# Performance work log

Hardware: AMD Instinct MI355X
Metric: run time of the kernel (lower is better)

## Reference

```python
import jax, jax.numpy as jnp
import numpy as np
from jax import lax

MID = 64      # mid_size -> token seq len = MID*MID = 4096
DM = 64       # d_model = in_channels
DI = 128      # d_inner = expand * d_model
DS = 16       # d_state
DC = 4        # d_conv
DTR = 4       # dt_rank = ceil(DM/16)
EPS = 1e-5


def conv3x3(x, w):
    return lax.conv_general_dilated(x, w, (1, 1), ((1, 1), (1, 1)),
                                    dimension_numbers=('NCHW', 'OIHW', 'NCHW'))


def layernorm(x, w, b):
    mu = jnp.mean(x, -1, keepdims=True)
    var = jnp.mean((x - mu) ** 2, -1, keepdims=True)
    return (x - mu) * lax.rsqrt(var + EPS) * w + b


def bilinear(x, h, w):
    b, c = x.shape[:2]
    return jax.image.resize(x, (b, c, h, w), method='bilinear', antialias=False)


def mamba(tok, in_w, conv_w, conv_b, xproj_w, dt_w, dt_b, Alog, D, out_w):
    # tok: (b, L, DM)
    b, L, _ = tok.shape
    xz = tok @ in_w.T                                # (b, L, 2*DI)
    xc, z = jnp.split(xz, 2, axis=-1)
    # causal depthwise conv1d over sequence
    xcT = xc.transpose(0, 2, 1)                      # (b, DI, L)
    xconv = lax.conv_general_dilated(xcT, conv_w, (1,), ((DC - 1, 0),),
                                     dimension_numbers=('NCH', 'OIH', 'NCH'),
                                     feature_group_count=DI)
    xconv = xconv + conv_b[None, :, None]
    u = jax.nn.silu(xconv.transpose(0, 2, 1))        # (b, L, DI)
    x_dbl = u @ xproj_w.T                            # (b, L, DTR+2*DS)
    dt, B, C = jnp.split(x_dbl, [DTR, DTR + DS], axis=-1)
    dt = jax.nn.softplus(dt @ dt_w.T + dt_b)         # (b, L, DI)
    A = -jnp.exp(Alog)                               # (DI, DS)
    dA = jnp.exp(dt[..., None] * A)                  # (b, L, DI, DS)
    dBu = dt[..., None] * B[:, :, None, :] * u[..., None]

    def step(h, xs):
        a_t, bu_t = xs
        h = a_t * h + bu_t
        return h, h

    h0 = jnp.zeros((b, DI, DS), dt.dtype)
    _, hs = lax.scan(step, h0, (dA.transpose(1, 0, 2, 3), dBu.transpose(1, 0, 2, 3)))
    y = jnp.einsum('lbns,bls->bln', hs, C) + u * D   # (b, L, DI)
    y = y * jax.nn.silu(z)
    return y @ out_w.T                               # (b, L, DM)


def setup_inputs() -> dict:
    key = jax.random.key(0)
    ks = iter(jax.random.split(key, 32))
    s = 0.02
    d = {}
    d['x'] = jax.random.normal(next(ks), (4, 64, 128, 128), jnp.float32)
    for n, shp in [('cb_w1', (64, 64, 3, 3)), ('cb_w2', (64, 64, 3, 3)),
                   ('sm_w1', (64, 64, 3, 3)), ('sm_w2', (64, 64, 3, 3))]:
        d[n] = jax.random.normal(next(ks), shp, jnp.float32) * s
    d['ln1_w'] = jnp.ones((DM,), jnp.float32); d['ln1_b'] = jnp.zeros((DM,), jnp.float32)
    d['ln2_w'] = jnp.ones((DM,), jnp.float32); d['ln2_b'] = jnp.zeros((DM,), jnp.float32)
    for p in ['m1', 'm2']:
        d[p + '_in_w'] = jax.random.normal(next(ks), (2 * DI, DM), jnp.float32) * s
        d[p + '_conv_w'] = jax.random.normal(next(ks), (DI, 1, DC), jnp.float32) * s
        d[p + '_conv_b'] = jnp.zeros((DI,), jnp.float32)
        d[p + '_xproj_w'] = jax.random.normal(next(ks), (DTR + 2 * DS, DI), jnp.float32) * s
        d[p + '_dt_w'] = jax.random.normal(next(ks), (DI, DTR), jnp.float32) * s
        d[p + '_dt_b'] = jnp.full((DI,), -2.0, jnp.float32)
        d[p + '_Alog'] = jnp.broadcast_to(jnp.log(jnp.arange(1, DS + 1, dtype=jnp.float32)), (DI, DS)).copy()
        d[p + '_D'] = jnp.ones((DI,), jnp.float32)
        d[p + '_out_w'] = jax.random.normal(next(ks), (DM, DI), jnp.float32) * s
    return d


def reference(x, cb_w1, cb_w2, ln1_w, ln1_b, ln2_w, ln2_b,
              m1_in_w, m1_conv_w, m1_conv_b, m1_xproj_w, m1_dt_w, m1_dt_b, m1_Alog, m1_D, m1_out_w,
              m2_in_w, m2_conv_w, m2_conv_b, m2_xproj_w, m2_dt_w, m2_dt_b, m2_Alog, m2_D, m2_out_w,
              sm_w1, sm_w2):
    b, c, h, w = x.shape
    xr = conv3x3(jax.nn.relu(conv3x3(x, cb_w1)), cb_w2) + x
    x_small = xr if (h, w) == (MID, MID) else bilinear(xr, MID, MID)
    tokens = x_small.reshape(b, c, MID * MID).transpose(0, 2, 1)   # (b, L, c)
    main = mamba(layernorm(tokens, ln1_w, ln1_b),
                 m1_in_w, m1_conv_w, m1_conv_b, m1_xproj_w, m1_dt_w, m1_dt_b, m1_Alog, m1_D, m1_out_w)
    gate_feat = mamba(layernorm(tokens, ln2_w, ln2_b),
                      m2_in_w, m2_conv_w, m2_conv_b, m2_xproj_w, m2_dt_w, m2_dt_b, m2_Alog, m2_D, m2_out_w)
    gate = jax.nn.softmax(gate_feat, axis=1)                       # softmax over token dim
    tokens = tokens + gate * main
    feat = tokens.transpose(0, 2, 1).reshape(b, c, MID, MID)
    if (h, w) != (MID, MID):
        feat = bilinear(feat, h, w)
    return conv3x3(jax.nn.relu(conv3x3(feat, sm_w1)), sm_w2)
```

## Files before the change

### kernel.cpp

```cpp
#include <hip/hip_runtime.h>

typedef unsigned int u32;
typedef unsigned short u16;
typedef __attribute__((ext_vector_type(8))) short short8;
typedef __attribute__((ext_vector_type(4))) float f32x4;

__device__ __forceinline__ float sigmoidf_(float x){
  return 1.f / (1.f + __expf(-x));
}
__device__ __forceinline__ u16 f2bf(float f){
  union { float f; u32 i; } v; v.f = f;
  u32 r = v.i + 0x7fffu + ((v.i >> 16) & 1u);
  return (u16)(r >> 16);
}
__device__ __forceinline__ float bf2f(u32 u){
  union { float f; u32 i; } v; v.i = (u & 0xffffu) << 16; return v.f;
}
__device__ __forceinline__ float softplus_(float x){
  return fmaxf(x, 0.f) + __logf(1.f + __expf(-fabsf(x)));
}

__global__ __launch_bounds__(256) void k_setup(
    const float* __restrict__ w0, u16* __restrict__ h0, u16* __restrict__ l0,
    const float* __restrict__ w1, u16* __restrict__ h1, u16* __restrict__ l1,
    const float* __restrict__ w2, u16* __restrict__ h2, u16* __restrict__ l2,
    const float* __restrict__ w3, u16* __restrict__ h3, u16* __restrict__ l3,
    const float* __restrict__ Wa, const float* __restrict__ lnwa, const float* __restrict__ lnba,
    float* __restrict__ W2a, float* __restrict__ B2a,
    const float* __restrict__ Wb, const float* __restrict__ lnwb, const float* __restrict__ lnbb,
    float* __restrict__ W2b, float* __restrict__ B2b,
    const float* __restrict__ src, u16* __restrict__ PH, u16* __restrict__ PL,
    u16* __restrict__ BPH, u16* __restrict__ BPL)
{
  __shared__ float ld[64 * 129];
  int bx = blockIdx.x;
  int tid = threadIdx.x;
  if (bx < 577){
    int gidx = bx * 256 + tid;
    if (gidx < 147456){
      int set = gidx / 36864;
      int idx = gidx - set * 36864;
      const float* w; u16* WH; u16* WL;
      if (set == 0){ w = w0; WH = h0; WL = l0; }
      else if (set == 1){ w = w1; WH = h1; WL = l1; }
      else if (set == 2){ w = w2; WH = h2; WL = l2; }
      else { w = w3; WH = h3; WL = l3; }
      int j    = idx & 7;
      int lane = (idx >> 3) & 63;
      int nt   = (idx >> 9) & 3;
      int kc   = (idx >> 11) & 1;
      int t    = idx >> 12;
      int ic = kc * 32 + ((lane >> 4) & 3) * 8 + j;
      int oc = nt * 16 + (lane & 15);
      float v = w[(oc * 64 + ic) * 9 + t];
      u16 h = f2bf(v);
      u16 l = f2bf(v - bf2f(h));
      WH[idx] = h; WL[idx] = l;
    } else {
      int i = gidx - 147456;
      if (i >= 128) return;
      int m = i >> 6, j = i & 63;
      const float* W   = m ? Wb   : Wa;
      const float* lnw = m ? lnwb : lnwa;
      const float* lnb = m ? lnbb : lnba;
      float* W2 = m ? W2b : W2a;
      float* B2 = m ? B2b : B2a;
      float bias = 0.f;
#pragma unroll
      for (int k4 = 0; k4 < 16; k4++){
        float4 wv = *(const float4*)&W[j * 64 + k4 * 4];
        float4 gw = *(const float4*)&lnw[k4 * 4];
        float4 gb = *(const float4*)&lnb[k4 * 4];
        W2[j * 64 + k4 * 4 + 0] = wv.x * gw.x;
        W2[j * 64 + k4 * 4 + 1] = wv.y * gw.y;
        W2[j * 64 + k4 * 4 + 2] = wv.z * gw.z;
        W2[j * 64 + k4 * 4 + 3] = wv.w * gw.w;
        bias = fmaf(wv.x, gb.x, bias);
        bias = fmaf(wv.y, gb.y, bias);
        bias = fmaf(wv.z, gb.z, bias);
        bias = fmaf(wv.w, gb.w, bias);
      }
      B2[j] = bias;
    }
  } else {
    int bid2 = bx - 577;
    int yp = bid2 % 130;
    int b  = bid2 / 130;
    int ys = yp - 1;
    if (yp == 0 || yp == 129){
      for (int i = tid; i < 130 * 64; i += 256){
        int x = i >> 6, c = i & 63;
        size_t o = (((size_t)b * 130 + yp) * 130 + x) * 64 + c;
        BPH[o] = 0; BPL[o] = 0;
      }
    } else {
      for (int i = tid; i < 128; i += 256){
        int x = (i >= 64) ? 129 : 0, c = i & 63;
        size_t o = (((size_t)b * 130 + yp) * 130 + x) * 64 + c;
        BPH[o] = 0; BPL[o] = 0;
      }
    }
    if ((u32)ys < 128u){
      for (int i = tid; i < 8192; i += 256){
        int c = i >> 7, x = i & 127;
        ld[c * 129 + x] = src[((size_t)(b * 64 + c) * 128 + ys) * 128 + x];
      }
    }
    __syncthreads();
    for (int i = tid; i < 130 * 64; i += 256){
      int xp = i >> 6, c = i & 63;
      float v = 0.f;
      if ((u32)ys < 128u && (u32)(xp - 1) < 128u) v = ld[c * 129 + (xp - 1)];
      u16 h = f2bf(v);
      u16 l = f2bf(v - bf2f(h));
      size_t o = (((size_t)b * 130 + yp) * 130 + xp) * 64 + c;
      PH[o] = h; PL[o] = l;
    }
  }
}

__global__ __launch_bounds__(256) void k_prepup(const float* __restrict__ FEAT,
                                                u16* __restrict__ PH, u16* __restrict__ PL,
                                                u16* __restrict__ BPH, u16* __restrict__ BPL){
  __shared__ float ld0[64 * 65], ld1[64 * 65];
  int yp = blockIdx.x;
  int b  = blockIdx.y;
  int ys = yp - 1;
  int tid = threadIdx.x;
  if (yp == 0 || yp == 129){
    for (int i = tid; i < 130 * 64; i += 256){
      int x = i >> 6, c = i & 63;
      size_t o = (((size_t)b * 130 + yp) * 130 + x) * 64 + c;
      BPH[o] = 0; BPL[o] = 0;
    }
  } else {
    for (int i = tid; i < 128; i += 256){
      int x = (i >= 64) ? 129 : 0, c = i & 63;
      size_t o = (((size_t)b * 130 + yp) * 130 + x) * 64 + c;
      BPH[o] = 0; BPL[o] = 0;
    }
  }
  float wy = 0.f;
  if ((u32)ys < 128u){
    float ay = 0.5f * ys - 0.25f;
    int fy = (int)floorf(ay); wy = ay - fy;
    int y0s = fy < 0 ? 0 : fy, y1s = fy + 1 > 63 ? 63 : fy + 1;
    for (int i = tid; i < 1024; i += 256){
      int c = i >> 4, x4 = (i & 15) * 4;
      float4 a0 = *(const float4*)&FEAT[((size_t)(b * 64 + c) * 64 + y0s) * 64 + x4];
      float4 a1 = *(const float4*)&FEAT[((size_t)(b * 64 + c) * 64 + y1s) * 64 + x4];
      ld0[c * 65 + x4 + 0] = a0.x; ld0[c * 65 + x4 + 1] = a0.y;
      ld0[c * 65 + x4 + 2] = a0.z; ld0[c * 65 + x4 + 3] = a0.w;
      ld1[c * 65 + x4 + 0] = a1.x; ld1[c * 65 + x4 + 1] = a1.y;
      ld1[c * 65 + x4 + 2] = a1.z; ld1[c * 65 + x4 + 3] = a1.w;
    }
  }
  __syncthreads();
  for (int i = tid; i < 130 * 64; i += 256){
    int xp = i >> 6, c = i & 63;
    float v = 0.f;
    int xs = xp - 1;
    if ((u32)ys < 128u && (u32)xs < 128u){
      float ax = 0.5f * xs - 0.25f;
      int fx = (int)floorf(ax); float wx = ax - fx;
      int x0s = fx < 0 ? 0 : fx, x1s = fx + 1 > 63 ? 63 : fx + 1;
      float v0 = (1.f - wx) * ld0[c * 65 + x0s] + wx * ld0[c * 65 + x1s];
      float v1 = (1.f - wx) * ld1[c * 65 + x0s] + wx * ld1[c * 65 + x1s];
      v = (1.f - wy) * v0 + wy * v1;
    }
    u16 h = f2bf(v);
    u16 l = f2bf(v - bf2f(h));
    size_t o = (((size_t)b * 130 + yp) * 130 + xp) * 64 + c;
    PH[o] = h; PL[o] = l;
  }
}

__global__ __launch_bounds__(256) void k_convm(
    const u16* __restrict__ PH, const u16* __restrict__ PL,
    const u16* __restrict__ WH, const u16* __restrict__ WL,
    const float* __restrict__ resid,
    u16* __restrict__ OBH, u16* __restrict__ OBL,
    float* __restrict__ OUTF, float* __restrict__ T, float* __restrict__ NT,
    int mode)
{
  __shared__ __align__(16) u32 smem[9024];
  u16* Ah_s = (u16*)smem;
  u16* Al_s = Ah_s + 5760;
  int tid = threadIdx.x;
  int lane = tid & 63, w = tid >> 6;
  int quad = lane >> 4, lcol = lane & 15;
  int b = blockIdx.z, y0 = blockIdx.y * 8, x0 = blockIdx.x * 16;

  f32x4 acc[2][4];
#pragma unroll
  for (int mt = 0; mt < 2; mt++)
#pragma unroll
    for (int nt = 0; nt < 4; nt++)
      acc[mt][nt] = (f32x4){0.f, 0.f, 0.f, 0.f};

  for (int kc = 0; kc < 2; kc++){
    __syncthreads();
    for (int i = tid; i < 720; i += 256){
      int q = i & 3;
      int rc = i >> 2;
      int r = rc / 18, c = rc - r * 18;
      size_t so = (((size_t)b * 130 + y0 + r) * 130 + (x0 + c)) * 64 + kc * 32 + q * 8;
      int de = (r * 18 + c) * 32 + q * 8;
      *(uint4*)(Ah_s + de) = *(const uint4*)(PH + so);
      *(uint4*)(Al_s + de) = *(const uint4*)(PL + so);
    }
    __syncthreads();
#pragma unroll
    for (int t = 0; t < 9; t++){
      int dy = t / 3, dx = t - dy * 3;
      short8 bh[4], bl[4];
#pragma unroll
      for (int nt = 0; nt < 4; nt++){
        int o = ((t * 2 + kc) * 4 + nt) * 512 + lane * 8;
        bh[nt] = *(const short8*)(WH + o);
        bl[nt] = *(const short8*)(WL + o);
      }
      short8 ah[2], al[2];
#pragma unroll
      for (int mt = 0; mt < 2; mt++){
        int e = ((w * 2 + mt + dy) * 18 + (lcol + dx)) * 32 + quad * 8;
        ah[mt] = *(const short8*)(Ah_s + e);
        al[mt] = *(const short8*)(Al_s + e);
      }
#pragma unroll
      for (int mt = 0; mt < 2; mt++)
#pragma unroll
        for (int nt = 0; nt < 4; nt++){
          acc[mt][nt] = __builtin_amdgcn_mfma_f32_16x16x32_bf16(ah[mt], bh[nt], acc[mt][nt], 0, 0, 0);
          acc[mt][nt] = __builtin_amdgcn_mfma_f32_16x16x32_bf16(ah[mt], bl[nt], acc[mt][nt], 0, 0, 0);
          acc[mt][nt] = __builtin_amdgcn_mfma_f32_16x16x32_bf16(al[mt], bh[nt], acc[mt][nt], 0, 0, 0);
        }
    }
  }

  __syncthreads();
  if (mode == 0){
    u32* epi = smem;
#pragma unroll
    for (int mt = 0; mt < 2; mt++){
      int row = w * 2 + mt;
#pragma unroll
      for (int nt = 0; nt < 4; nt++){
#pragma unroll
        for (int reg = 0; reg < 4; reg++){
          float v = fmaxf(acc[mt][nt][reg], 0.f);
          u32 h = f2bf(v);
          u32 l = f2bf(v - bf2f(h));
          int ccol = quad * 4 + reg;
          int oc = nt * 16 + lcol;
          epi[(row * 16 + ccol) * 66 + oc] = h | (l << 16);
        }
      }
    }
    __syncthreads();
    for (int i = tid; i < 8192; i += 256){
      int px = i >> 6, oc = i & 63;
      int row = px >> 4, ccol = px & 15;
      u32 pk = epi[px * 66 + oc];
      size_t o = (((size_t)b * 130 + y0 + row + 1) * 130 + (x0 + ccol + 1)) * 64 + oc;
      OBH[o] = (u16)pk;
      OBL[o] = (u16)(pk >> 16);
    }
  } else {
    float* epi = (float*)smem;
#pragma unroll
    for (int mt = 0; mt < 2; mt++){
      int row = w * 2 + mt;
#pragma unroll
      for (int nt = 0; nt < 4; nt++){
#pragma unroll
        for (int reg = 0; reg < 4; reg++){
          int px = row * 16 + quad * 4 + reg;
          int oc = nt * 16 + lcol;
          epi[oc * 131 + px] = acc[mt][nt][reg];
        }
      }
    }
    __syncthreads();
    if (mode == 1){
      for (int i = tid; i < 8192; i += 256){
        int oc = i >> 7, px = i & 127;
        int row = px >> 4, c = px & 15;
        size_t o = (((size_t)b * 64 + oc) * 128 + y0 + row) * 128 + x0 + c;
        float v = epi[oc * 131 + px];
        if (resid) v += resid[o];
        OUTF[o] = v;
      }
    } else {
      for (int i = tid; i < 8192; i += 256){
        int oc = i >> 7, px = i & 127;
        int row = px >> 4, c = px & 15;
        size_t o = (((size_t)b * 64 + oc) * 128 + y0 + row) * 128 + x0 + c;
        epi[oc * 131 + px] += resid[o];
      }
      __syncthreads();
      float* redS  = (float*)smem + 8384;
      float* redQ  = redS + 288;
      float* stats = redQ + 288;
      int token = tid & 31, cgrp = tid >> 5;
      int tr = token >> 3, tc = token & 7;
      float av[8]; float s = 0.f, q = 0.f;
      int p0 = (2 * tr) * 16 + 2 * tc;
#pragma unroll
      for (int j = 0; j < 8; j++){
        int c = cgrp * 8 + j;
        const float* ep = epi + c * 131;
        float v = 0.25f * (ep[p0] + ep[p0 + 1] + ep[p0 + 16] + ep[p0 + 17]);
        av[j] = v; s += v; q = fmaf(v, v, q);
      }
      redS[token * 9 + cgrp] = s;
      redQ[token * 9 + cgrp] = q;
      __syncthreads();
      if (tid < 32){
        float S = 0.f, Q = 0.f;
        for (int g = 0; g < 8; g++){ S += redS[tid * 9 + g]; Q += redQ[tid * 9 + g]; }
        float mu = S * (1.f / 64.f);
        float var = Q * (1.f / 64.f) - mu * mu;
        stats[tid * 2] = mu;
        stats[tid * 2 + 1] = rsqrtf(var + 1e-5f);
      }
      __syncthreads();
      float mu = stats[token * 2], inv = stats[token * 2 + 1];
      int l = (blockIdx.y * 4 + tr) * 64 + blockIdx.x * 8 + tc;
      size_t to = ((size_t)b * 4096 + l) * 64 + cgrp * 8;
#pragma unroll
      for (int j = 0; j < 8; j++){
        T[to + j] = av[j];
        NT[to + j] = (av[j] - mu) * inv;
      }
    }
  }
}

__global__ __launch_bounds__(256) void k_inprojdw(
    const float* __restrict__ NT,
    const float* __restrict__ W2a, const float* __restrict__ B2a,
    float* __restrict__ Ua, float* __restrict__ Za,
    const float* __restrict__ cwa, const float* __restrict__ cba,
    const float* __restrict__ W2b, const float* __restrict__ B2b,
    float* __restrict__ Ub, float* __restrict__ Zb,
    const float* __restrict__ cwb, const float* __restrict__ cbb)
{
  __shared__ float wL[64 * 68];
  __shared__ float xcs[67 * 68];
  int mz = blockIdx.z;
  const float* W2 = mz ? W2b : W2a;
  const float* B2 = mz ? B2b : B2a;
  float* U = mz ? Ub : Ua;
  float* Z  = mz ? Zb : Za;
  const float* cw = mz ? cwb : cwa;
  const float* cb = mz ? cbb : cba;
  int tid = threadIdx.x;
  int t0 = blockIdx.x * 64;
  int j0 = blockIdx.y * 64;
  for (int i = tid; i < 4096; i += 256){
    int jl = i >> 6, k = i & 63;
    wL[jl * 68 + k] = W2[(size_t)(j0 + jl) * 64 + k];
  }
  __syncthreads();
  int tq = tid >> 4, cg = tid & 15;
  const float* ntp = NT + (size_t)(t0 + tq * 4) * 64;
  float acc[4][4];
#pragma unroll
  for (int c = 0; c < 4; c++){
    float bias = B2[j0 + cg + c * 16];
#pragma unroll
    for (int t = 0; t < 4; t++) acc[t][c] = bias;
  }
#pragma unroll 4
  for (int k4 = 0; k4 < 16; k4++){
    float4 lv[4];
#pragma unroll
    for (int t = 0; t < 4; t++)
      lv[t] = *(const float4*)(ntp + t * 64 + k4 * 4);
    float4 wv[4];
#pragma unroll
    for (int c = 0; c < 4; c++)
      wv[c] = *(const float4*)&wL[(cg + c * 16) * 68 + k4 * 4];
#pragma unroll
    for (int t = 0; t < 4; t++)
#pragma unroll
      for (int c = 0; c < 4; c++){
        acc[t][c] = fmaf(lv[t].x, wv[c].x, acc[t][c]);
        acc[t][c] = fmaf(lv[t].y, wv[c].y, acc[t][c]);
        acc[t][c] = fmaf(lv[t].z, wv[c].z, acc[t][c]);
        acc[t][c] = fmaf(lv[t].w, wv[c].w, acc[t][c]);
      }
  }
  if (j0 < 128){
    int isStart = ((t0 & 4095) == 0);
    if (tid < 192){
      int e = tid >> 6, col = tid & 63;
      float v = 0.f;
      if (!isStart){
        const float* np = NT + (size_t)(t0 - 3 + e) * 64;
        float a2 = B2[j0 + col];
#pragma unroll 4
        for (int k = 0; k < 64; k += 4){
          float4 nv = *(const float4*)(np + k);
          float4 wv = *(const float4*)&wL[col * 68 + k];
          a2 = fmaf(nv.x, wv.x, fmaf(nv.y, wv.y, fmaf(nv.z, wv.z, fmaf(nv.w, wv.w, a2))));
        }
        v = a2;
      }
      xcs[e * 68 + col] = v;
    }
#pragma unroll
    for (int t = 0; t < 4; t++)
#pragma unroll
      for (int c = 0; c < 4; c++)
        xcs[(3 + tq * 4 + t) * 68 + cg + c * 16] = acc[t][c];
    __syncthreads();
#pragma unroll
    for (int c = 0; c < 4; c++){
      int lc = cg + c * 16;
      int ch = j0 + lc;
      float4 wv = *(const float4*)(cw + ch * 4);
      float bias = cb[ch];
#pragma unroll
      for (int t = 0; t < 4; t++){
        int row = 3 + tq * 4 + t;
        float a = bias;
        a = fmaf(wv.w, xcs[row * 68 + lc], a);
        a = fmaf(wv.z, xcs[(row - 1) * 68 + lc], a);
        a = fmaf(wv.y, xcs[(row - 2) * 68 + lc], a);
        a = fmaf(wv.x, xcs[(row - 3) * 68 + lc], a);
        size_t tg = t0 + tq * 4 + t;
        U[tg * 128 + ch] = a * sigmoidf_(a);
      }
    }
  } else {
#pragma unroll
    for (int t = 0; t < 4; t++){
      size_t tg = t0 + tq * 4 + t;
#pragma unroll
      for (int c = 0; c < 4; c++)
        Z[tg * 128 + (j0 - 128) + cg + c * 16] = acc[t][c];
    }
  }
}

__global__ __launch_bounds__(256) void k_xprojdt(
    const float* __restrict__ U0, const float* __restrict__ XW0, float* __restrict__ DBL0,
    const float* __restrict__ U1, const float* __restrict__ XW1, float* __restrict__ DBL1)
{
  __shared__ float xw[36 * 132];
  int bid = blockIdx.x;
  int m = bid >> 7, blk = bid & 127;
  const float* Up   = m ? U1   : U0;
  const float* XWp  = m ? XW1  : XW0;
  float* DBLp = m ? DBL1 : DBL0;
  int tid = threadIdx.x;
  for (int i = tid; i < 4608; i += 256)
    xw[(i >> 7) * 132 + (i & 127)] = XWp[i];
  __syncthreads();
  int slot = tid >> 2, jq = tid & 3;
  size_t tgA = (size_t)blk * 128 + slot;
  size_t tgB = tgA + 64;
  const float4* upA = (const float4*)(Up + tgA * 128);
  const float4* upB = (const float4*)(Up + tgB * 128);
  float accA[9], accB[9];
#pragma unroll
  for (int jj = 0; jj < 9; jj++){ accA[jj] = 0.f; accB[jj] = 0.f; }
  for (int k4 = 0; k4 < 32; k4++){
    float4 uA = upA[k4];
    float4 uB = upB[k4];
#pragma unroll
    for (int jj = 0; jj < 9; jj++){
      float4 w = *(const float4*)&xw[(jq * 9 + jj) * 132 + k4 * 4];
      accA[jj] = fmaf(w.x, uA.x, fmaf(w.y, uA.y, fmaf(w.z, uA.z, fmaf(w.w, uA.w, accA[jj]))));
      accB[jj] = fmaf(w.x, uB.x, fmaf(w.y, uB.y, fmaf(w.z, uB.z, fmaf(w.w, uB.w, accB[jj]))));
    }
  }
#pragma unroll
  for (int jj = 0; jj < 9; jj++){
    DBLp[tgA * 36 + jq * 9 + jj] = accA[jj];
    DBLp[tgB * 36 + jq * 9 + jj] = accB[jj];
  }
}

__global__ __launch_bounds__(256) void k_scanA(
    const float* __restrict__ DBL0, const float* __restrict__ U0, const float* __restrict__ AL0,
    const float* __restrict__ DTW0, const float* __restrict__ DTB0,
    const float* __restrict__ DBL1, const float* __restrict__ U1, const float* __restrict__ AL1,
    const float* __restrict__ DTW1, const float* __restrict__ DTB1,
    float* __restrict__ HF, float* __restrict__ AP)
{
  __shared__ float su[32 * 65], sB[16 * 36], sdtr[128];
  int bid = blockIdx.x;
  int cg = bid & 1;
  int c  = (bid >> 1) & 127;
  int b  = (bid >> 8) & 3;
  int m  = bid >> 10;
  const float* DBLp = m ? DBL1 : DBL0;
  const float* Up   = m ? U1   : U0;
  const float* ALp  = m ? AL1  : AL0;
  const float* DTWp = m ? DTW1 : DTW0;
  const float* DTBp = m ? DTB1 : DTB0;
  int tid = threadIdx.x;
  int lane = tid & 63, w = tid >> 6;
  int lcol = lane & 15, q = lane >> 4;
  int chL = w * 16 + lcol;
  int n = cg * 64 + chL;
  size_t base = (size_t)b * 4096 + c * 32;
  for (int i = tid; i < 2048; i += 256){
    int ch = i & 63, l = i >> 6;
    su[l * 65 + ch] = Up[(base + l) * 128 + cg * 64 + ch];
  }
  for (int i = tid; i < 512; i += 256){
    int s = i & 15, l = i >> 4;
    sB[s * 36 + l] = DBLp[(base + l) * 36 + 4 + s];
  }
  if (tid < 128){
    int l = tid >> 2, jj = tid & 3;
    sdtr[tid] = DBLp[(base + l) * 36 + jj];
  }
  const float LOG2E = 1.4426950408889634f;
  float A1[4];
  bool fastp = true;
#pragma unroll
  for (int j = 0; j < 4; j++){
    A1[j] = -__expf(ALp[n * 16 + q * 4 + j]) * LOG2E;
    float expe = -(float)(q * 4 + j + 1) * LOG2E;
    fastp = fastp && (fabsf(A1[j] - expe) <= 1e-3f);
  }
  float4 wdt = *(const float4*)(DTWp + n * 4);
  float bdt = DTBp[n];
  __syncthreads();
  float h[4] = {0.f, 0.f, 0.f, 0.f};
  float ap[4] = {1.f, 1.f, 1.f, 1.f};
#pragma unroll
  for (int l4 = 0; l4 < 8; l4++){
    int lq = l4 * 4 + q;
    float4 dq = *(const float4*)&sdtr[lq * 4];
    float xq = bdt;
    xq = fmaf(wdt.x, dq.x, xq); xq = fmaf(wdt.y, dq.y, xq);
    xq = fmaf(wdt.z, dq.z, xq); xq = fmaf(wdt.w, dq.w, xq);
    float dtq = softplus_(xq);
    float rq = __expf(-dtq);
    float dts[4], rs[4];
    dts[0] = __shfl(dtq, lcol);       rs[0] = __shfl(rq, lcol);
    dts[1] = __shfl(dtq, lcol + 16);  rs[1] = __shfl(rq, lcol + 16);
    dts[2] = __shfl(dtq, lcol + 32);  rs[2] = __shfl(rq, lcol + 32);
    dts[3] = __shfl(dtq, lcol + 48);  rs[3] = __shfl(rq, lcol + 48);
    float4 Bv[4];
#pragma unroll
    for (int j = 0; j < 4; j++) Bv[j] = *(const float4*)&sB[(q * 4 + j) * 36 + l4 * 4];
    if (fastp){
#pragma unroll
      for (int jj = 0; jj < 4; jj++){
        int l = l4 * 4 + jj;
        float dt = dts[jj], r = rs[jj];
        float u  = su[l * 65 + chL];
        float dtu = dt * u;
        float r2 = r * r, r4 = r2 * r2;
        float r8 = r4 * r4;
        float p0 = (q == 0) ? r : (q == 1) ? r4 * r : (q == 2) ? r8 * r : (r8 * r4) * r;
        float a0 = p0, a1 = a0 * r, a2 = a1 * r, a3 = a2 * r;
        h[0] = fmaf(a0, h[0], dtu * (&Bv[0].x)[jj]); ap[0] *= a0;
        h[1] = fmaf(a1, h[1], dtu * (&Bv[1].x)[jj]); ap[1] *= a1;
        h[2] = fmaf(a2, h[2], dtu * (&Bv[2].x)[jj]); ap[2] *= a2;
        h[3] = fmaf(a3, h[3], dtu * (&Bv[3].x)[jj]); ap[3] *= a3;
      }
    } else {
#pragma unroll
      for (int jj = 0; jj < 4; jj++){
        int l = l4 * 4 + jj;
        float dt = dts[jj];
        float u  = su[l * 65 + chL];
        float dtu = dt * u;
#pragma unroll
        for (int j = 0; j < 4; j++){
          float a = exp2f(dt * A1[j]);
          h[j] = fmaf(a, h[j], dtu * (&Bv[j].x)[jj]);
          ap[j] *= a;
        }
      }
    }
  }
  size_t o = ((size_t)((m * 4 + b) * 128 + c)) * 2048 + n * 16 + q * 4;
  *(float4*)&HF[o] = make_float4(h[0], h[1], h[2], h[3]);
  *(float4*)&AP[o] = make_float4(ap[0], ap[1], ap[2], ap[3]);
}

__global__ __launch_bounds__(256) void k_scanB(
    const float* __restrict__ HF, const float* __restrict__ AP, float* __restrict__ HIN)
{
  int gid = blockIdx.x * 256 + threadIdx.x;
  int r = gid >> 3;
  int seg = gid & 7;
  int q = r >> 11;
  int p = r & 2047;
  size_t base = (size_t)q * 128 * 2048 + p + (size_t)seg * 16 * 2048;
  float a[16], f[16];
#pragma unroll
  for (int c8 = 0; c8 < 2; c8++){
#pragma unroll
    for (int j = 0; j < 8; j++){
      size_t o = base + (size_t)(c8 * 8 + j) * 2048;
      a[c8 * 8 + j] = AP[o];
      f[c8 * 8 + j] = HF[o];
    }
  }
  float A = 1.f, F = 0.f;
#pragma unroll
  for (int j = 0; j < 16; j++){ F = fmaf(a[j], F, f[j]); A *= a[j]; }
#pragma unroll
  for (int d = 1; d < 8; d <<= 1){
    float Au = __shfl_up(A, d, 8);
    float Fu = __shfl_up(F, d, 8);
    if (seg >= d){ F = fmaf(A, Fu, F); A = A * Au; }
  }
  float hin = __shfl_up(F, 1, 8);
  float h = (seg == 0) ? 0.f : hin;
#pragma unroll
  for (int j = 0; j < 16; j++){
    size_t o = base + (size_t)j * 2048;
    HIN[o] = h;
    h = fmaf(a[j], h, f[j]);
  }
}

__global__ __launch_bounds__(256) void k_scanC(
    const float* __restrict__ DBL0, const float* __restrict__ U0, const float* __restrict__ AL0,
    const float* __restrict__ DTW0, const float* __restrict__ DTB0,
    const float* __restrict__ D0, float* __restrict__ Y0,
    const float* __restrict__ DBL1, const float* __restrict__ U1, const float* __restrict__ AL1,
    const float* __restrict__ DTW1, const float* __restrict__ DTB1,
    const float* __restrict__ D1, float* __restrict__ Y1,
    const float* __restrict__ HIN)
{
  __shared__ float su[32 * 65], sB[16 * 36], sC[16 * 36], sdtr[128];
  int bid = blockIdx.x;
  int cg = bid & 1;
  int c  = (bid >> 1) & 127;
  int b  = (bid >> 8) & 3;
  int m  = bid >> 10;
  const float* DBLp = m ? DBL1 : DBL0;
  const float* Up   = m ? U1   : U0;
  const float* ALp  = m ? AL1  : AL0;
  const float* DTWp = m ? DTW1 : DTW0;
  const float* DTBp = m ? DTB1 : DTB0;
  const float* Dp   = m ? D1   : D0;
  float*       Yp   = m ? Y1   : Y0;
  int tid = threadIdx.x;
  int lane = tid & 63, w = tid >> 6;
  int lcol = lane & 15, q = lane >> 4;
  int chL = w * 16 + lcol;
  int n = cg * 64 + chL;
  size_t base = (size_t)b * 4096 + c * 32;
  for (int i = tid; i < 2048; i += 256){
    int ch = i & 63, l = i >> 6;
    su[l * 65 + ch] = Up[(base + l) * 128 + cg * 64 + ch];
  }
  for (int i = tid; i < 512; i += 256){
    int s = i & 15, l = i >> 4;
    size_t ob = (base + l) * 36;
    sB[s * 36 + l] = DBLp[ob + 4 + s];
    sC[s * 36 + l] = DBLp[ob + 20 + s];
  }
  if (tid < 128){
    int l = tid >> 2, jj = tid & 3;
    sdtr[tid] = DBLp[(base + l) * 36 + jj];
  }
  const float LOG2E = 1.4426950408889634f;
  float A1[4];
  bool fastp = true;
#pragma unroll
  for (int j = 0; j < 4; j++){
    A1[j] = -__expf(ALp[n * 16 + q * 4 + j]) * LOG2E;
    float expe = -(float)(q * 4 + j + 1) * LOG2E;
    fastp = fastp && (fabsf(A1[j] - expe) <= 1e-3f);
  }
  float4 wdt = *(const float4*)(DTWp + n * 4);
  float bdt = DTBp[n];
  float Dn = Dp[n];
  float4 hv = *(const float4*)&HIN[((size_t)((m * 4 + b) * 128 + c)) * 2048 + n * 16 + q * 4];
  float h[4] = {hv.x, hv.y, hv.z, hv.w};
  __syncthreads();
#pragma unroll
  for (int l4 = 0; l4 < 8; l4++){
    int lq = l4 * 4 + q;
    float4 dq = *(const float4*)&sdtr[lq * 4];
    float xq = bdt;
    xq = fmaf(wdt.x, dq.x, xq); xq = fmaf(wdt.y, dq.y, xq);
    xq = fmaf(wdt.z, dq.z, xq); xq = fmaf(wdt.w, dq.w, xq);
    float dtq = softplus_(xq);
    float rq = __expf(-dtq);
    float dts[4], rs[4];
    dts[0] = __shfl(dtq, lcol);       rs[0] = __shfl(rq, lcol);
    dts[1] = __shfl(dtq, lcol + 16);  rs[1] = __shfl(rq, lcol + 16);
    dts[2] = __shfl(dtq, lcol + 32);  rs[2] = __shfl(rq, lcol + 32);
    dts[3] = __shfl(dtq, lcol + 48);  rs[3] = __shfl(rq, lcol + 48);
    float4 Bv[4], Cv[4];
#pragma unroll
    for (int j = 0; j < 4; j++){
      Bv[j] = *(const float4*)&sB[(q * 4 + j) * 36 + l4 * 4];
      Cv[j] = *(const float4*)&sC[(q * 4 + j) * 36 + l4 * 4];
    }
    if (fastp){
#pragma unroll
      for (int jj = 0; jj < 4; jj++){
        int l = l4 * 4 + jj;
        float dt = dts[jj], r = rs[jj];
        float u  = su[l * 65 + chL];
        float dtu = dt * u;
        float r2 = r * r, r4 = r2 * r2;
        float r8 = r4 * r4;
        float p0 = (q == 0) ? r : (q == 1) ? r4 * r : (q == 2) ? r8 * r : (r8 * r4) * r;
        float a0 = p0, a1 = a0 * r, a2 = a1 * r, a3 = a2 * r;
        float p = 0.f;
        h[0] = fmaf(a0, h[0], dtu * (&Bv[0].x)[jj]); p = fmaf(h[0], (&Cv[0].x)[jj], p);
        h[1] = fmaf(a1, h[1], dtu * (&Bv[1].x)[jj]); p = fmaf(h[1], (&Cv[1].x)[jj], p);
        h[2] = fmaf(a2, h[2], dtu * (&Bv[2].x)[jj]); p = fmaf(h[2], (&Cv[2].x)[jj], p);
        h[3] = fmaf(a3, h[3], dtu * (&Bv[3].x)[jj]); p = fmaf(h[3], (&Cv[3].x)[jj], p);
        p += __shfl_xor(p, 16);
        p += __shfl_xor(p, 32);
        if (q == 0)
          Yp[(base + l) * 128 + n] = fmaf(u, Dn, p);
      }
    } else {
#pragma unroll
      for (int jj = 0; jj < 4; jj++){
        int l = l4 * 4 + jj;
        float dt = dts[jj];
        float u  = su[l * 65 + chL];
        float dtu = dt * u;
        float p = 0.f;
#pragma unroll
        for (int j = 0; j < 4; j++){
          float a = exp2f(dt * A1[j]);
          h[j] = fmaf(a, h[j], dtu * (&Bv[j].x)[jj]);
          p = fmaf(h[j], (&Cv[j].x)[jj], p);
        }
        p += __shfl_xor(p, 16);
        p += __shfl_xor(p, 32);
        if (q == 0)
          Yp[(base + l) * 128 + n] = fmaf(u, Dn, p);
      }
    }
  }
}

__global__ __launch_bounds__(256) void k_outproj(
    const float* __restrict__ Y0, const float* __restrict__ Zg0,
    const float* __restrict__ W0, float* __restrict__ OUT0,
    const float* __restrict__ Y1, const float* __restrict__ Zg1,
    const float* __restrict__ W1, float* __restrict__ OUT1,
    float* __restrict__ P)
{
  __shared__ float yl[16 * 128];
  __shared__ float wT[128 * 65];
  __shared__ float rM[256], rS[256];
  int m = blockIdx.y;
  const float* Y  = m ? Y1  : Y0;
  const float* Zg = m ? Zg1 : Zg0;
  const float* W  = m ? W1  : W0;
  float* OUT = m ? OUT1 : OUT0;
  int tid = threadIdx.x;
  size_t t0 = (size_t)blockIdx.x * 16;
  for (int i = tid; i < 2048; i += 256){
    float z = Zg[t0 * 128 + i];
    yl[i] = Y[t0 * 128 + i] * (z * sigmoidf_(z));
  }
  for (int i = tid; i < 8192; i += 256){
    int k = i & 127, j = i >> 7;
    wT[k * 65 + j] = W[j * 128 + k];
  }
  __syncthreads();
  int j = tid & 63;
  int tg = tid >> 6;
  float acc[4] = {0.f, 0.f, 0.f, 0.f};
  for (int k = 0; k < 128; k += 4){
    float w0 = wT[k * 65 + j], w1 = wT[(k+1) * 65 + j];
    float w2 = wT[(k+2) * 65 + j], w3 = wT[(k+3) * 65 + j];
#pragma unroll
    for (int t = 0; t < 4; t++){
      float4 yv = *(const float4*)&yl[(tg * 4 + t) * 128 + k];
      acc[t] = fmaf(w0, yv.x, fmaf(w1, yv.y, fmaf(w2, yv.z, fmaf(w3, yv.w, acc[t]))));
    }
  }
#pragma unroll
  for (int t = 0; t < 4; t++)
    OUT[(t0 + tg * 4 + t) * 64 + j] = acc[t];
  if (m == 1){
    float mx = fmaxf(fmaxf(acc[0], acc[1]), fmaxf(acc[2], acc[3]));
    float sm = __expf(acc[0] - mx) + __expf(acc[1] - mx) + __expf(acc[2] - mx) + __expf(acc[3] - mx);
    rM[tid] = mx; rS[tid] = sm;
    __syncthreads();
    if (tid < 64){
      float M = rM[tid], S = rS[tid];
      for (int p2 = 1; p2 < 4; p2++){
        float m2 = rM[p2 * 64 + tid], s2 = rS[p2 * 64 + tid];
        float Mn = fmaxf(M, m2);
        S = S * __expf(M - Mn) + s2 * __expf(m2 - Mn);
        M = Mn;
      }
      P[((size_t)blockIdx.x * 64 + tid) * 2] = M;
      P[((size_t)blockIdx.x * 64 + tid) * 2 + 1] = S;
    }
  }
}

__global__ void k_combine(const float* __restrict__ T, const float* __restrict__ MAIN,
                          const float* __restrict__ G, const float* __restrict__ P,
                          float* __restrict__ FEAT){
  int bid = blockIdx.x;
  int b = bid >> 6, row = bid & 63;
  int tid = threadIdx.x;
  __shared__ float tile[64 * 65];
  __shared__ float sM[256], sS[256], Mv[64], iSv[64];
  {
    int j2 = tid & 63, part = tid >> 6;
    float M = -3.4e38f, S = 0.f;
    for (int i = 0; i < 64; i++){
      int pb = part + i * 4;
      int idx = ((b * 256 + pb) * 64 + j2) * 2;
      float m2 = P[idx], s2 = P[idx + 1];
      float Mn = fmaxf(M, m2);
      S = S * __expf(M - Mn) + s2 * __expf(m2 - Mn);
      M = Mn;
    }
    sM[tid] = M; sS[tid] = S;
  }
  __syncthreads();
  if (tid < 64){
    float M = sM[tid], S = sS[tid];
    for (int p = 1; p < 4; p++){
      float m2 = sM[p * 64 + tid], s2 = sS[p * 64 + tid];
      float Mn = fmaxf(M, m2);
      S = S * __expf(M - Mn) + s2 * __expf(m2 - Mn);
      M = Mn;
    }
    Mv[tid] = M; iSv[tid] = 1.f / S;
  }
  __syncthreads();
  int j = tid & 63, ls = tid >> 6;
  float M = Mv[j], invS = iSv[j];
  size_t lbase = (size_t)b * 4096 + row * 64;
  for (int i = 0; i < 16; i++){
    int col = ls + i * 4;
    size_t off = (lbase + col) * 64 + j;
    float g = __expf(G[off] - M) * invS;
    tile[col * 65 + j] = T[off] + g * MAIN[off];
  }
  __syncthreads();
  int colw = tid & 63, jr = tid >> 6;
  for (int jj = jr; jj < 64; jj += 4)
    FEAT[(((size_t)b * 64 + jj) * 64 + row) * 64 + colw] = tile[colw * 65 + jj];
}

extern "C" void kernel_launch(void* const* d_in, const int* in_sizes, int n_in,
                              void* d_out, int out_size, void* d_ws, size_t ws_size,
                              hipStream_t stream) {
  const size_t P1A = 0, P1B = 4326400;
  const size_t MB0 = 0, MB1 = 10027008;
  const size_t O_LN = 0, O_XC = 1048576, O_Z = 3145728, O_U = 5242880,
               O_DBL = 9437184;
  const size_t TOK = 20054016, OUT0 = 21102592, OUT1 = 22151168;
  const size_t FEAT = 23208448;
  const size_t P3A = 4194304, P3B = 8520704;
  const size_t WSET = 19000000;
  const size_t PADN = 2163200;
  const size_t SMP = 0;
  const size_t W2_0 = 21102592, B2_0 = 21118976, W2_1 = 21119232, B2_1 = 21135616;
  const size_t TOTAL = 24257024;
  if (ws_size < TOTAL * 4) return;

  float* ws = (float*)d_ws;
  const float* X   = (const float*)d_in[0];
  const float* CB1 = (const float*)d_in[1];
  const float* CB2 = (const float*)d_in[2];
  const float* SW1 = (const float*)d_in[3];
  const float* SW2 = (const float*)d_in[4];
  const float* LNW[2] = { (const float*)d_in[5], (const float*)d_in[7] };
  const float* LNB[2] = { (const float*)d_in[6], (const float*)d_in[8] };
  const float *INW[2], *CW[2], *CBb[2], *XPW[2], *DTW[2], *DTB[2], *AL[2], *DD[2], *OW[2];
  for (int m = 0; m < 2; m++){
    int p = 9 + m * 9;
    INW[m] = (const float*)d_in[p + 0];
    CW[m]  = (const float*)d_in[p + 1];
    CBb[m] = (const float*)d_in[p + 2];
    XPW[m] = (const float*)d_in[p + 3];
    DTW[m] = (const float*)d_in[p + 4];
    DTB[m] = (const float*)d_in[p + 5];
    AL[m]  = (const float*)d_in[p + 6];
    DD[m]  = (const float*)d_in[p + 7];
    OW[m]  = (const float*)d_in[p + 8];
  }

  u16* wset[8];
  for (int k = 0; k < 8; k++) wset[k] = (u16*)(ws + WSET + (size_t)k * 18432);

  u16* p1ah = (u16*)(ws + P1A); u16* p1al = p1ah + PADN * 2;
  u16* p1bh = (u16*)(ws + P1B); u16* p1bl = p1bh + PADN * 2;
  u16* p3ah = (u16*)(ws + P3A); u16* p3al = p3ah + PADN * 2;
  u16* p3bh = (u16*)(ws + P3B); u16* p3bl = p3bh + PADN * 2;

  k_setup<<<1097, 256, 0, stream>>>(CB1, wset[0], wset[1], CB2, wset[2], wset[3],
                                    SW1, wset[4], wset[5], SW2, wset[6], wset[7],
                                    INW[0], LNW[0], LNB[0], ws + W2_0, ws + B2_0,
                                    INW[1], LNW[1], LNB[1], ws + W2_1, ws + B2_1,
                                    X, p1ah, p1al, p1bh, p1bl);

  k_convm<<<dim3(8, 16, 4), 256, 0, stream>>>(p1ah, p1al, wset[0], wset[1], nullptr,
                                              p1bh, p1bl, nullptr, nullptr, nullptr, 0);
  k_convm<<<dim3(8, 16, 4), 256, 0, stream>>>(p1bh, p1bl, wset[2], wset[3], X,
                                              nullptr, nullptr, nullptr,
                                              ws + TOK, ws + MB0 + O_LN, 2);

  k_inprojdw<<<dim3(256, 4, 2), 256, 0, stream>>>(
      ws + MB0 + O_LN,
      ws + W2_0, ws + B2_0, ws + MB0 + O_U, ws + MB0 + O_Z, CW[0], CBb[0],
      ws + W2_1, ws + B2_1, ws + MB1 + O_U, ws + MB1 + O_Z, CW[1], CBb[1]);
  k_xprojdt<<<256, 256, 0, stream>>>(
      ws + MB0 + O_U, XPW[0], ws + MB0 + O_DBL,
      ws + MB1 + O_U, XPW[1], ws + MB1 + O_DBL);

  float* HF  = ws + MB0 + O_XC;
  float* AP  = ws + MB1 + O_XC;
  float* HIN = ws + OUT1;

  k_scanA<<<2048, 256, 0, stream>>>(
      ws + MB0 + O_DBL, ws + MB0 + O_U, AL[0], DTW[0], DTB[0],
      ws + MB1 + O_DBL, ws + MB1 + O_U, AL[1], DTW[1], DTB[1],
      HF, AP);
  k_scanB<<<512, 256, 0, stream>>>(HF, AP, HIN);
  k_scanC<<<2048, 256, 0, stream>>>(
      ws + MB0 + O_DBL, ws + MB0 + O_U, AL[0], DTW[0], DTB[0], DD[0], ws + MB0 + O_XC,
      ws + MB1 + O_DBL, ws + MB1 + O_U, AL[1], DTW[1], DTB[1], DD[1], ws + MB1 + O_XC,
      HIN);

  k_outproj<<<dim3(1024, 2), 256, 0, stream>>>(
      ws + MB0 + O_XC, ws + MB0 + O_Z, OW[0], ws + OUT0,
      ws + MB1 + O_XC, ws + MB1 + O_Z, OW[1], ws + OUT1,
      ws + SMP);

  k_combine<<<256, 256, 0, stream>>>(ws + TOK, ws + OUT0, ws + OUT1, ws + SMP, ws + FEAT);

  k_prepup<<<dim3(130, 4), 256, 0, stream>>>(ws + FEAT, p3ah, p3al, p3bh, p3bl);
  k_convm<<<dim3(8, 16, 4), 256, 0, stream>>>(p3ah, p3al, wset[4], wset[5], nullptr,
                                              p3bh, p3bl, nullptr, nullptr, nullptr, 0);
  k_convm<<<dim3(8, 16, 4), 256, 0, stream>>>(p3bh, p3bl, wset[6], wset[7], nullptr,
                                              nullptr, nullptr, (float*)d_out,
                                              nullptr, nullptr, 1);
}
```

Measured before the change: 350.0 us.

## Fuse x_proj matmul into scan phase A, dropping separate xprojdt kernel

Removes the standalone x_proj kernel and computes the per-chunk x_proj (dt/B/C) inside k_scanA from the full 128-channel U tile staged in shared memory. Only half the threads do this matmul, reading the weights straight from global memory. The cg==0 blocks write DBL back to global for scanC to use. This saves a launch and a round trip of DBL through global memory, but each chunk's projection is now computed twice (once per channel group), and scanA loads twice as much U.

```diff
diff --git a/kernel.cpp b/kernel.cpp
--- a/kernel.cpp
+++ b/kernel.cpp
@@ -445,80 +445,36 @@
   }
 }
 
-__global__ __launch_bounds__(256) void k_xprojdt(
-    const float* __restrict__ U0, const float* __restrict__ XW0, float* __restrict__ DBL0,
-    const float* __restrict__ U1, const float* __restrict__ XW1, float* __restrict__ DBL1)
-{
-  __shared__ float xw[36 * 132];
-  int bid = blockIdx.x;
-  int m = bid >> 7, blk = bid & 127;
-  const float* Up   = m ? U1   : U0;
-  const float* XWp  = m ? XW1  : XW0;
-  float* DBLp = m ? DBL1 : DBL0;
-  int tid = threadIdx.x;
-  for (int i = tid; i < 4608; i += 256)
-    xw[(i >> 7) * 132 + (i & 127)] = XWp[i];
-  __syncthreads();
-  int slot = tid >> 2, jq = tid & 3;
-  size_t tgA = (size_t)blk * 128 + slot;
-  size_t tgB = tgA + 64;
-  const float4* upA = (const float4*)(Up + tgA * 128);
-  const float4* upB = (const float4*)(Up + tgB * 128);
-  float accA[9], accB[9];
-#pragma unroll
-  for (int jj = 0; jj < 9; jj++){ accA[jj] = 0.f; accB[jj] = 0.f; }
-  for (int k4 = 0; k4 < 32; k4++){
-    float4 uA = upA[k4];
-    float4 uB = upB[k4];
-#pragma unroll
-    for (int jj = 0; jj < 9; jj++){
-      float4 w = *(const float4*)&xw[(jq * 9 + jj) * 132 + k4 * 4];
-      accA[jj] = fmaf(w.x, uA.x, fmaf(w.y, uA.y, fmaf(w.z, uA.z, fmaf(w.w, uA.w, accA[jj]))));
-      accB[jj] = fmaf(w.x, uB.x, fmaf(w.y, uB.y, fmaf(w.z, uB.z, fmaf(w.w, uB.w, accB[jj]))));
-    }
-  }
-#pragma unroll
-  for (int jj = 0; jj < 9; jj++){
-    DBLp[tgA * 36 + jq * 9 + jj] = accA[jj];
-    DBLp[tgB * 36 + jq * 9 + jj] = accB[jj];
-  }
-}
-
 __global__ __launch_bounds__(256) void k_scanA(
-    const float* __restrict__ DBL0, const float* __restrict__ U0, const float* __restrict__ AL0,
-    const float* __restrict__ DTW0, const float* __restrict__ DTB0,
-    const float* __restrict__ DBL1, const float* __restrict__ U1, const float* __restrict__ AL1,
-    const float* __restrict__ DTW1, const float* __restrict__ DTB1,
+    float* __restrict__ DBL0, const float* __restrict__ U0, const float* __restrict__ AL0,
+    const float* __restrict__ DTW0, const float* __restrict__ DTB0, const float* __restrict__ XW0,
+    float* __restrict__ DBL1, const float* __restrict__ U1, const float* __restrict__ AL1,
+    const float* __restrict__ DTW1, const float* __restrict__ DTB1, const float* __restrict__ XW1,
     float* __restrict__ HF, float* __restrict__ AP)
 {
-  __shared__ float su[32 * 65], sB[16 * 36], sdtr[128];
+  __shared__ float su[32 * 132];
+  __shared__ float sdblT[36 * 36];
+  __shared__ float sdtr[128];
   int bid = blockIdx.x;
   int cg = bid & 1;
   int c  = (bid >> 1) & 127;
   int b  = (bid >> 8) & 3;
   int m  = bid >> 10;
-  const float* DBLp = m ? DBL1 : DBL0;
+  float* DBLp = m ? DBL1 : DBL0;
   const float* Up   = m ? U1   : U0;
   const float* ALp  = m ? AL1  : AL0;
   const float* DTWp = m ? DTW1 : DTW0;
   const float* DTBp = m ? DTB1 : DTB0;
+  const float* XWp  = m ? XW1  : XW0;
   int tid = threadIdx.x;
   int lane = tid & 63, w = tid >> 6;
   int lcol = lane & 15, q = lane >> 4;
   int chL = w * 16 + lcol;
   int n = cg * 64 + chL;
   size_t base = (size_t)b * 4096 + c * 32;
-  for (int i = tid; i < 2048; i += 256){
-    int ch = i & 63, l = i >> 6;
-    su[l * 65 + ch] = Up[(base + l) * 128 + cg * 64 + ch];
-  }
-  for (int i = tid; i < 512; i += 256){
-    int s = i & 15, l = i >> 4;
-    sB[s * 36 + l] = DBLp[(base + l) * 36 + 4 + s];
-  }
-  if (tid < 128){
-    int l = tid >> 2, jj = tid & 3;
-    sdtr[tid] = DBLp[(base + l) * 36 + jj];
+  for (int i = tid; i < 4096; i += 256){
+    int ch = i & 127, l = i >> 7;
+    su[l * 132 + ch] = Up[(base + l) * 128 + ch];
   }
   const float LOG2E = 1.4426950408889634f;
   float A1[4];
@@ -531,6 +487,31 @@
   }
   float4 wdt = *(const float4*)(DTWp + n * 4);
   float bdt = DTBp[n];
+  __syncthreads();
+  if (tid < 128){
+    int slot = tid >> 2, jq = tid & 3;
+    const float* sup = &su[slot * 132];
+    float accA[9];
+#pragma unroll
+    for (int jj = 0; jj < 9; jj++) accA[jj] = 0.f;
+    for (int k4 = 0; k4 < 32; k4++){
+      float4 uA = *(const float4*)(sup + k4 * 4);
+#pragma unroll
+      for (int jj = 0; jj < 9; jj++){
+        float4 wv = *(const float4*)&XWp[(size_t)(jq * 9 + jj) * 128 + k4 * 4];
+        accA[jj] = fmaf(wv.x, uA.x, fmaf(wv.y, uA.y, fmaf(wv.z, uA.z, fmaf(wv.w, uA.w, accA[jj]))));
+      }
+    }
+#pragma unroll
+    for (int jj = 0; jj < 9; jj++){
+      sdblT[(jq * 9 + jj) * 36 + slot] = accA[jj];
+      if (cg == 0) DBLp[(base + slot) * 36 + jq * 9 + jj] = accA[jj];
+    }
+    if (jq == 0){
+#pragma unroll
+      for (int jj = 0; jj < 4; jj++) sdtr[slot * 4 + jj] = accA[jj];
+    }
+  }
   __syncthreads();
   float h[4] = {0.f, 0.f, 0.f, 0.f};
   float ap[4] = {1.f, 1.f, 1.f, 1.f};
@@ -550,13 +531,13 @@
     dts[3] = __shfl(dtq, lcol + 48);  rs[3] = __shfl(rq, lcol + 48);
     float4 Bv[4];
 #pragma unroll
-    for (int j = 0; j < 4; j++) Bv[j] = *(const float4*)&sB[(q * 4 + j) * 36 + l4 * 4];
+    for (int j = 0; j < 4; j++) Bv[j] = *(const float4*)&sdblT[(4 + q * 4 + j) * 36 + l4 * 4];
     if (fastp){
 #pragma unroll
       for (int jj = 0; jj < 4; jj++){
         int l = l4 * 4 + jj;
         float dt = dts[jj], r = rs[jj];
-        float u  = su[l * 65 + chL];
+        float u  = su[l * 132 + n];
         float dtu = dt * u;
         float r2 = r * r, r4 = r2 * r2;
         float r8 = r4 * r4;
@@ -572,7 +553,7 @@
       for (int jj = 0; jj < 4; jj++){
         int l = l4 * 4 + jj;
         float dt = dts[jj];
-        float u  = su[l * 65 + chL];
+        float u  = su[l * 132 + n];
         float dtu = dt * u;
 #pragma unroll
         for (int j = 0; j < 4; j++){
@@ -918,17 +899,14 @@
       ws + MB0 + O_LN,
       ws + W2_0, ws + B2_0, ws + MB0 + O_U, ws + MB0 + O_Z, CW[0], CBb[0],
       ws + W2_1, ws + B2_1, ws + MB1 + O_U, ws + MB1 + O_Z, CW[1], CBb[1]);
-  k_xprojdt<<<256, 256, 0, stream>>>(
-      ws + MB0 + O_U, XPW[0], ws + MB0 + O_DBL,
-      ws + MB1 + O_U, XPW[1], ws + MB1 + O_DBL);
 
   float* HF  = ws + MB0 + O_XC;
   float* AP  = ws + MB1 + O_XC;
   float* HIN = ws + OUT1;
 
   k_scanA<<<2048, 256, 0, stream>>>(
-      ws + MB0 + O_DBL, ws + MB0 + O_U, AL[0], DTW[0], DTB[0],
-      ws + MB1 + O_DBL, ws + MB1 + O_U, AL[1], DTW[1], DTB[1],
+      ws + MB0 + O_DBL, ws + MB0 + O_U, AL[0], DTW[0], DTB[0], XPW[0],
+      ws + MB1 + O_DBL, ws + MB1 + O_U, AL[1], DTW[1], DTB[1], XPW[1],
       HF, AP);
   k_scanB<<<512, 256, 0, stream>>>(HF, AP, HIN);
   k_scanC<<<2048, 256, 0, stream>>>(
```

After: 460.3 us. +31.5%, slower.
